# Kernel optimization log

Hardware: AMD Instinct MI355X
Metric: run time of the kernel (lower is better)

The kernel has to match this reference:

```python
import jax, jax.numpy as jnp
import numpy as np

B, L, D, H, HID = 2048, 512, 17, 8, 256  # batch, max entities, feat dim, heads, mlp hidden
SPECIAL, OUT = 9, 23  # special vector dims, policy logits (7+16)


def _lin(k, out_d, in_d, scale):
    kw, kb = jax.random.split(k)
    W = jax.random.normal(kw, (out_d, in_d), jnp.float32) * scale
    b = jax.random.normal(kb, (out_d,), jnp.float32) * 0.01
    return W, b


def setup_inputs() -> dict:
    key = jax.random.key(0)
    ks = jax.random.split(key, 16)
    # observations: row 0 holds the 9-dim special vector, rows 1..L are ragged entities
    x = jax.random.normal(ks[0], (B, L + 1, D), jnp.float32)
    lengths = jax.random.randint(ks[1], (B,), 1, L + 1)
    mask = (jnp.arange(L)[None, :] < lengths[:, None]).astype(jnp.float32)
    x = x.at[:, 1:, :].multiply(mask[:, :, None])  # zero rows mark padding
    s = 1.0 / np.sqrt(D)
    # per-head K/V projections (num_heads separate tiny Linears)
    Wk = jax.random.normal(ks[2], (H, D, D), jnp.float32) * s
    bk = jax.random.normal(ks[3], (H, D), jnp.float32) * 0.01
    Wv = jax.random.normal(ks[4], (H, D, D), jnp.float32) * s
    bv = jax.random.normal(ks[5], (H, D), jnp.float32) * 0.01
    q = jax.random.normal(ks[6], (H, D), jnp.float32)  # learned per-head queries
    Wo, bo = _lin(ks[7], D, H * D, 1.0 / np.sqrt(H * D))
    sc = 1.0 / np.sqrt(D + SPECIAL)
    pW1, pb1 = _lin(ks[8], HID, D + SPECIAL, sc)
    pW2, pb2 = _lin(ks[9], HID, HID, 1.0 / np.sqrt(HID))
    pW3, pb3 = _lin(ks[10], OUT, HID, 1.0 / np.sqrt(HID))
    vW1, vb1 = _lin(ks[11], HID, D + SPECIAL, sc)
    vW2, vb2 = _lin(ks[12], HID, HID, 1.0 / np.sqrt(HID))
    vW3, vb3 = _lin(ks[13], 1, HID, 1.0 / np.sqrt(HID))
    return dict(x=x, Wk=Wk, bk=bk, Wv=Wv, bv=bv, q=q, Wo=Wo, bo=bo,
                pW1=pW1, pb1=pb1, pW2=pW2, pb2=pb2, pW3=pW3, pb3=pb3,
                vW1=vW1, vb1=vb1, vW2=vW2, vb2=vb2, vW3=vW3, vb3=vb3)


def _mlp(h, W1, b1, W2, b2, W3, b3):
    h = jax.nn.relu(h @ W1.T + b1)
    h = jax.nn.relu(h @ W2.T + b2)
    return h @ W3.T + b3


def reference(x, Wk, bk, Wv, bv, q, Wo, bo,
              pW1, pb1, pW2, pb2, pW3, pb3,
              vW1, vb1, vW2, vb2, vW3, vb3):
    special = x[:, 0, :SPECIAL]            # [B, 9]
    seq = x[:, 1:, :]                      # [B, L, D]
    mask = jnp.sum(jnp.abs(seq), axis=-1) != 0  # [B, L] non-padded rows
    # per-head keys/values for all samples at once (batched over the head loop)
    keys = jnp.einsum('bld,hed->bhle', seq, Wk) + bk[None, :, None, :]   # [B,H,L,D]
    vals = jnp.einsum('bld,hed->bhle', seq, Wv) + bv[None, :, None, :]   # [B,H,L,D]
    scores = jnp.einsum('bhle,he->bhl', keys, q)                          # [B,H,L]
    scores = jnp.where(mask[:, None, :], scores, -1e9)
    w = jax.nn.softmax(scores, axis=-1)                                   # [B,H,L]
    agg = jnp.einsum('bhl,bhle->bhe', w, vals).reshape(x.shape[0], H * D)  # concat heads
    attn = agg @ Wo.T + bo                                                # [B, D]
    comb = jnp.concatenate([attn, special], axis=-1)                      # [B, D+9]
    logits = _mlp(comb, pW1, pb1, pW2, pb2, pW3, pb3)                     # [B, 23]
    value = _mlp(comb, vW1, vb1, vW2, vb2, vW3, vb3)                      # [B, 1]
    return logits, value
```

## Files before the change

kernel.cpp:

```cpp
#include <hip/hip_runtime.h>
#include <hip/hip_bf16.h>

#define B_ 2048
#define D_ 17
#define H_ 8
#define HID_ 256
#define OUT_ 23
#define XROW 8721
#define SEQN 8704
#define LAST4 4465151

typedef unsigned int u32;
typedef const __attribute__((address_space(1))) u32* gp1_t;
typedef __attribute__((address_space(3))) u32* lp3_t;

__device__ __forceinline__ float bclane(float v, int l) {
  return __uint_as_float(__builtin_amdgcn_readlane(__float_as_uint(v), l));
}

__device__ __forceinline__ void gload_lds16(const float4* gsrc_lane, float* lds_wave_base) {
  __builtin_amdgcn_global_load_lds((gp1_t)(const void*)gsrc_lane,
                                   (lp3_t)(void*)lds_wave_base, 16, 0, 0);
}

__global__ __launch_bounds__(256) void prep_kernel(
    const float* __restrict__ pW2, const float* __restrict__ vW2,
    const float* __restrict__ Wk, const float* __restrict__ bk,
    const float* __restrict__ q,
    float* __restrict__ pW2t, float* __restrict__ vW2t, float* __restrict__ qkc)
{
  const int bid = blockIdx.x;
  const int t = threadIdx.x;
  if (bid == 128) {
    if (t < H_ * D_) {
      const int h = t / D_, dd = t - h * D_;
      float s = 0.f;
      #pragma unroll
      for (int e = 0; e < D_; ++e) s = fmaf(Wk[h*289 + e*D_ + dd], q[h*D_ + e], s);
      qkc[h*18 + dd] = s;
    } else if (t < H_ * D_ + H_) {
      const int h = t - H_ * D_;
      float s = 0.f;
      #pragma unroll
      for (int e = 0; e < D_; ++e) s = fmaf(bk[h*D_ + e], q[h*D_ + e], s);
      qkc[h*18 + 17] = s;
    }
    return;
  }
  __shared__ float tile[32][33];
  const int m = bid >> 6, tid = bid & 63;
  const int ti = (tid >> 3) * 32, tk = (tid & 7) * 32;
  const float* src = m ? vW2 : pW2;
  float* dst = m ? vW2t : pW2t;
  const int tx = t & 31, ty = t >> 5;
  #pragma unroll
  for (int r = 0; r < 4; ++r) tile[ty + 8*r][tx] = src[(ti + ty + 8*r)*HID_ + tk + tx];
  __syncthreads();
  #pragma unroll
  for (int r = 0; r < 4; ++r) dst[(tk + ty + 8*r)*HID_ + ti + tx] = tile[tx][ty + 8*r];
}

__global__ __launch_bounds__(256, 4) void attn_comb_kernel(
    const float* __restrict__ x, const float* __restrict__ qkc,
    const float* __restrict__ Wv, const float* __restrict__ bv,
    const float* __restrict__ Wo, const float* __restrict__ bo,
    float* __restrict__ comb)
{
  __shared__ __align__(16) float s_seq[9216];
  __shared__ float s_part[4][H_][18];
  __shared__ float s_swn[136];
  __shared__ float s_agg[136];
  __shared__ float s_wp[136];

  const int t = threadIdx.x;
  const int b = blockIdx.x;
  const int w = t >> 6, lane = t & 63;
  const int hp = lane >> 4;
  const int rg = lane & 15;
  const int seq0 = b * XROW + D_;
  const int s4 = seq0 >> 2;
  const int phase = seq0 & 3;
  const float4* __restrict__ x4 = (const float4*)x;

  const float pv = x[seq0 + lane * 136];

  {
    float* dstb = s_seq + ((t & ~63) << 2);
    const int g0 = s4 + t;
    gload_lds16(x4 + g0,          dstb);
    gload_lds16(x4 + g0 + 256,    dstb + 1024);
    gload_lds16(x4 + g0 + 512,    dstb + 2048);
    gload_lds16(x4 + g0 + 768,    dstb + 3072);
    gload_lds16(x4 + g0 + 1024,   dstb + 4096);

    const unsigned long long live = __ballot(pv != 0.f) | 1ull;
    const int nr = 8 * (64 - __builtin_clzll(live));
    const int rounds = min(9, (nr * D_ + phase + 1023) >> 10);

    if (rounds > 5) gload_lds16(x4 + g0 + 1280, dstb + 5120);
    if (rounds > 6) gload_lds16(x4 + g0 + 1536, dstb + 6144);
    if (rounds > 7) gload_lds16(x4 + g0 + 1792, dstb + 7168);
    if (rounds > 8) gload_lds16(x4 + min(g0 + 2048, LAST4), dstb + 8192);
  }
  const unsigned long long live2 = __ballot(pv != 0.f) | 1ull;
  const int nrows = 8 * (64 - __builtin_clzll(live2));

  const float* q0 = qkc + (2*hp) * 18;
  float qk0[D_], qk1[D_];
  #pragma unroll
  for (int d = 0; d < D_; ++d) { qk0[d] = q0[d]; qk1[d] = q0[18 + d]; }
  const float ch0 = q0[17], ch1 = q0[35];

  __syncthreads();

  float den0 = 0.f, den1 = 0.f;
  float acc0[D_], acc1[D_];
  #pragma unroll
  for (int d = 0; d < D_; ++d) { acc0[d] = 0.f; acc1[d] = 0.f; }

  auto dorow = [&](int row) {
    const float* rp = &s_seq[phase + row * D_];
    const float f0 = rp[0],  f1 = rp[1],  f2 = rp[2],  f3 = rp[3];
    const float f4 = rp[4],  f5 = rp[5],  f6 = rp[6],  f7 = rp[7];
    const float f8 = rp[8],  f9 = rp[9],  f10 = rp[10], f11 = rp[11];
    const float f12 = rp[12], f13 = rp[13], f14 = rp[14], f15 = rp[15];
    const float f16 = rp[16];
    float sA = ch0, sB = ch1;
    sA = fmaf(qk0[0],  f0,  sA); sB = fmaf(qk1[0],  f0,  sB);
    sA = fmaf(qk0[1],  f1,  sA); sB = fmaf(qk1[1],  f1,  sB);
    sA = fmaf(qk0[2],  f2,  sA); sB = fmaf(qk1[2],  f2,  sB);
    sA = fmaf(qk0[3],  f3,  sA); sB = fmaf(qk1[3],  f3,  sB);
    sA = fmaf(qk0[4],  f4,  sA); sB = fmaf(qk1[4],  f4,  sB);
    sA = fmaf(qk0[5],  f5,  sA); sB = fmaf(qk1[5],  f5,  sB);
    sA = fmaf(qk0[6],  f6,  sA); sB = fmaf(qk1[6],  f6,  sB);
    sA = fmaf(qk0[7],  f7,  sA); sB = fmaf(qk1[7],  f7,  sB);
    sA = fmaf(qk0[8],  f8,  sA); sB = fmaf(qk1[8],  f8,  sB);
    sA = fmaf(qk0[9],  f9,  sA); sB = fmaf(qk1[9],  f9,  sB);
    sA = fmaf(qk0[10], f10, sA); sB = fmaf(qk1[10], f10, sB);
    sA = fmaf(qk0[11], f11, sA); sB = fmaf(qk1[11], f11, sB);
    sA = fmaf(qk0[12], f12, sA); sB = fmaf(qk1[12], f12, sB);
    sA = fmaf(qk0[13], f13, sA); sB = fmaf(qk1[13], f13, sB);
    sA = fmaf(qk0[14], f14, sA); sB = fmaf(qk1[14], f14, sB);
    sA = fmaf(qk0[15], f15, sA); sB = fmaf(qk1[15], f15, sB);
    sA = fmaf(qk0[16], f16, sA); sB = fmaf(qk1[16], f16, sB);
    const bool lv = (row < nrows) && (f0 != 0.f);
    const float p0 = lv ? __expf(sA) : 0.f;
    const float p1 = lv ? __expf(sB) : 0.f;
    den0 += p0; den1 += p1;
    acc0[0]  = fmaf(p0, f0,  acc0[0]);  acc1[0]  = fmaf(p1, f0,  acc1[0]);
    acc0[1]  = fmaf(p0, f1,  acc0[1]);  acc1[1]  = fmaf(p1, f1,  acc1[1]);
    acc0[2]  = fmaf(p0, f2,  acc0[2]);  acc1[2]  = fmaf(p1, f2,  acc1[2]);
    acc0[3]  = fmaf(p0, f3,  acc0[3]);  acc1[3]  = fmaf(p1, f3,  acc1[3]);
    acc0[4]  = fmaf(p0, f4,  acc0[4]);  acc1[4]  = fmaf(p1, f4,  acc1[4]);
    acc0[5]  = fmaf(p0, f5,  acc0[5]);  acc1[5]  = fmaf(p1, f5,  acc1[5]);
    acc0[6]  = fmaf(p0, f6,  acc0[6]);  acc1[6]  = fmaf(p1, f6,  acc1[6]);
    acc0[7]  = fmaf(p0, f7,  acc0[7]);  acc1[7]  = fmaf(p1, f7,  acc1[7]);
    acc0[8]  = fmaf(p0, f8,  acc0[8]);  acc1[8]  = fmaf(p1, f8,  acc1[8]);
    acc0[9]  = fmaf(p0, f9,  acc0[9]);  acc1[9]  = fmaf(p1, f9,  acc1[9]);
    acc0[10] = fmaf(p0, f10, acc0[10]); acc1[10] = fmaf(p1, f10, acc1[10]);
    acc0[11] = fmaf(p0, f11, acc0[11]); acc1[11] = fmaf(p1, f11, acc1[11]);
    acc0[12] = fmaf(p0, f12, acc0[12]); acc1[12] = fmaf(p1, f12, acc1[12]);
    acc0[13] = fmaf(p0, f13, acc0[13]); acc1[13] = fmaf(p1, f13, acc1[13]);
    acc0[14] = fmaf(p0, f14, acc0[14]); acc1[14] = fmaf(p1, f14, acc1[14]);
    acc0[15] = fmaf(p0, f15, acc0[15]); acc1[15] = fmaf(p1, f15, acc1[15]);
    acc0[16] = fmaf(p0, f16, acc0[16]); acc1[16] = fmaf(p1, f16, acc1[16]);
  };

  {
    const int s0r = w * 64;
    if (s0r < nrows) {
      dorow(s0r + rg);
      dorow(s0r + rg + 16);
      dorow(s0r + rg + 32);
      dorow(s0r + rg + 48);
    }
    const int s1r = 256 + w * 64;
    if (s1r < nrows) {
      dorow(s1r + rg);
      dorow(s1r + rg + 16);
      dorow(s1r + rg + 32);
      dorow(s1r + rg + 48);
    }
  }

  #pragma unroll
  for (int m = 1; m <= 8; m <<= 1) {
    den0 += __shfl_xor(den0, m, 64);
    den1 += __shfl_xor(den1, m, 64);
    #pragma unroll
    for (int d = 0; d < D_; ++d) {
      acc0[d] += __shfl_xor(acc0[d], m, 64);
      acc1[d] += __shfl_xor(acc1[d], m, 64);
    }
  }
  if (rg == 0) {
    float* p0p = &s_part[w][2*hp][0];
    float* p1p = &s_part[w][2*hp + 1][0];
    p0p[0] = den0; p1p[0] = den1;
    #pragma unroll
    for (int d = 0; d < D_; ++d) { p0p[1 + d] = acc0[d]; p1p[1 + d] = acc1[d]; }
  }
  __syncthreads();

  if (t < 136) {
    const int hh = t / D_, d = t - hh * D_;
    float dn = 0.f, ac = 0.f;
    #pragma unroll
    for (int ww = 0; ww < 4; ++ww) { dn += s_part[ww][hh][0]; ac += s_part[ww][hh][1 + d]; }
    s_swn[t] = ac / dn;
  }
  __syncthreads();
  if (t < 136) {
    const int hh = t / D_, e = t - hh * D_;
    float s = bv[t];
    #pragma unroll
    for (int d = 0; d < D_; ++d) s = fmaf(Wv[hh*289 + e*D_ + d], s_swn[hh*D_ + d], s);
    s_agg[t] = s;
  }
  __syncthreads();
  if (t < 136) {
    const int o = t >> 3, pt = t & 7;
    float s = 0.f;
    #pragma unroll
    for (int j = 0; j < D_; ++j) s = fmaf(Wo[o*136 + pt*D_ + j], s_agg[pt*D_ + j], s);
    s_wp[t] = s;
  }
  __syncthreads();
  if (t < D_) {
    float s = bo[t];
    #pragma unroll
    for (int pt = 0; pt < 8; ++pt) s += s_wp[t*8 + pt];
    comb[b*26 + t] = s;
  } else if (t < 26) {
    comb[b*26 + t] = x[b * XROW + (t - D_)];
  }
}

__global__ __launch_bounds__(512) void mlp_kernel(
    const float* __restrict__ comb,
    const float* __restrict__ pW1, const float* __restrict__ pb1,
    const float* __restrict__ pW2t, const float* __restrict__ pb2,
    const float* __restrict__ pW3, const float* __restrict__ pb3,
    const float* __restrict__ vW1, const float* __restrict__ vb1,
    const float* __restrict__ vW2t, const float* __restrict__ vb2,
    const float* __restrict__ vW3, const float* __restrict__ vb3,
    float* __restrict__ out)
{
  __shared__ float s_comb[4][26];
  __shared__ __align__(16) float s_red[2][3][4][HID_];
  __shared__ __align__(16) float s_h2[2][4][HID_];

  const int t = threadIdx.x;
  const int b0 = blockIdx.x * 4;
  const int p = t >> 8;
  const int kq = (t >> 6) & 3;
  const int ln = t & 63;

  if (t < 104) { const int bb = t / 26, k = t - bb*26; s_comb[bb][k] = comb[(size_t)(b0 + bb)*26 + k]; }
  __syncthreads();

  const float* W1  = p ? vW1  : pW1;   const float* B1 = p ? vb1 : pb1;
  const float* W2t = p ? vW2t : pW2t;  const float* B2 = p ? vb2 : pb2;

  float h[4];
  {
    const int i = kq * 64 + ln;
    float a[4] = {0.f, 0.f, 0.f, 0.f};
    const float* wr = W1 + i * 26;
    for (int k = 0; k < 26; ++k) {
      const float wk = wr[k];
      #pragma unroll
      for (int bb = 0; bb < 4; ++bb) a[bb] = fmaf(wk, s_comb[bb][k], a[bb]);
    }
    const float bias = B1[i];
    #pragma unroll
    for (int bb = 0; bb < 4; ++bb) h[bb] = fmaxf(a[bb] + bias, 0.f);
  }

  float4 acc[4];
  #pragma unroll
  for (int bb = 0; bb < 4; ++bb) acc[bb] = make_float4(0.f, 0.f, 0.f, 0.f);
  {
    const float* wbase = W2t + (size_t)(kq * 64) * HID_ + 4 * ln;
    #pragma unroll 8
    for (int jj = 0; jj < 64; ++jj) {
      const float4 wv = *(const float4*)(wbase + (size_t)jj * HID_);
      #pragma unroll
      for (int bb = 0; bb < 4; ++bb) {
        const float hv = bclane(h[bb], jj);
        acc[bb].x = fmaf(wv.x, hv, acc[bb].x);
        acc[bb].y = fmaf(wv.y, hv, acc[bb].y);
        acc[bb].z = fmaf(wv.z, hv, acc[bb].z);
        acc[bb].w = fmaf(wv.w, hv, acc[bb].w);
      }
    }
  }
  if (kq > 0) {
    #pragma unroll
    for (int bb = 0; bb < 4; ++bb) *(float4*)&s_red[p][kq - 1][bb][4 * ln] = acc[bb];
  }
  __syncthreads();
  if (kq == 0) {
    const float4 bias = *(const float4*)&B2[4 * ln];
    #pragma unroll
    for (int bb = 0; bb < 4; ++bb) {
      const float4 r0 = *(const float4*)&s_red[p][0][bb][4 * ln];
      const float4 r1 = *(const float4*)&s_red[p][1][bb][4 * ln];
      const float4 r2 = *(const float4*)&s_red[p][2][bb][4 * ln];
      float4 rr;
      rr.x = fmaxf(acc[bb].x + r0.x + r1.x + r2.x + bias.x, 0.f);
      rr.y = fmaxf(acc[bb].y + r0.y + r1.y + r2.y + bias.y, 0.f);
      rr.z = fmaxf(acc[bb].z + r0.z + r1.z + r2.z + bias.z, 0.f);
      rr.w = fmaxf(acc[bb].w + r0.w + r1.w + r2.w + bias.w, 0.f);
      *(float4*)&s_h2[p][bb][4 * ln] = rr;
    }
  }
  __syncthreads();

  if (t < 92) {
    const int bb = t / OUT_, o = t - bb * OUT_;
    const float4* w4 = (const float4*)(pW3 + o * HID_);
    const float4* h4 = (const float4*)&s_h2[0][bb][0];
    float s = pb3[o];
    for (int k = 0; k < 64; ++k) {
      const float4 wv = w4[k], hv = h4[k];
      s = fmaf(wv.x, hv.x, fmaf(wv.y, hv.y, fmaf(wv.z, hv.z, fmaf(wv.w, hv.w, s))));
    }
    out[(size_t)(b0 + bb) * OUT_ + o] = s;
  } else if (t >= 256 && t < 260) {
    const int bb = t - 256;
    const float4* w4 = (const float4*)vW3;
    const float4* h4 = (const float4*)&s_h2[1][bb][0];
    float s = vb3[0];
    for (int k = 0; k < 64; ++k) {
      const float4 wv = w4[k], hv = h4[k];
      s = fmaf(wv.x, hv.x, fmaf(wv.y, hv.y, fmaf(wv.z, hv.z, fmaf(wv.w, hv.w, s))));
    }
    out[(size_t)B_ * OUT_ + b0 + bb] = s;
  }
}

extern "C" void kernel_launch(void* const* d_in, const int* in_sizes, int n_in,
                              void* d_out, int out_size, void* d_ws, size_t ws_size,
                              hipStream_t stream) {
  (void)in_sizes; (void)n_in; (void)out_size; (void)ws_size;
  const float* x   = (const float*)d_in[0];
  const float* Wk  = (const float*)d_in[1];
  const float* bk  = (const float*)d_in[2];
  const float* Wv  = (const float*)d_in[3];
  const float* bv  = (const float*)d_in[4];
  const float* q   = (const float*)d_in[5];
  const float* Wo  = (const float*)d_in[6];
  const float* bo  = (const float*)d_in[7];
  const float* pW1 = (const float*)d_in[8];
  const float* pb1 = (const float*)d_in[9];
  const float* pW2 = (const float*)d_in[10];
  const float* pb2 = (const float*)d_in[11];
  const float* pW3 = (const float*)d_in[12];
  const float* pb3 = (const float*)d_in[13];
  const float* vW1 = (const float*)d_in[14];
  const float* vb1 = (const float*)d_in[15];
  const float* vW2 = (const float*)d_in[16];
  const float* vb2 = (const float*)d_in[17];
  const float* vW3 = (const float*)d_in[18];
  const float* vb3 = (const float*)d_in[19];
  float* out = (float*)d_out;

  float* pW2t = (float*)d_ws;
  float* vW2t = pW2t + (size_t)HID_ * HID_;
  float* qkc  = vW2t + (size_t)HID_ * HID_;
  float* comb = qkc + 160;

  prep_kernel<<<129, 256, 0, stream>>>(pW2, vW2, Wk, bk, q, pW2t, vW2t, qkc);
  attn_comb_kernel<<<B_, 256, 0, stream>>>(x, qkc, Wv, bv, Wo, bo, comb);
  mlp_kernel<<<B_ / 4, 512, 0, stream>>>(comb, pW1, pb1, pW2t, pb2, pW3, pb3,
                                         vW1, vb1, vW2t, vb2, vW3, vb3, out);
}
```

Before: 53.35 us.

## Fuse attention pooling and MLP heads into one kernel over 4 samples

Merges the per-sample attention kernel and the batched MLP kernel into a single kernel. Each block loops over 4 samples to compute the combined features into shared memory, then runs the policy and value MLPs serially, reusing the sequence buffer. This removes one launch and the global round trip of the combined features. In exchange, the grid shrinks fourfold, loads for successive samples are serialized without overlap, and occupancy hints change, which may reduce memory-level parallelism.

```diff
diff --git a/kernel.cpp b/kernel.cpp
--- a/kernel.cpp
+++ b/kernel.cpp
@@ -60,184 +60,10 @@
   for (int r = 0; r < 4; ++r) dst[(tk + ty + 8*r)*HID_ + ti + tx] = tile[tx][ty + 8*r];
 }
 
-__global__ __launch_bounds__(256, 4) void attn_comb_kernel(
+__global__ __launch_bounds__(256, 3) void fused_kernel(
     const float* __restrict__ x, const float* __restrict__ qkc,
     const float* __restrict__ Wv, const float* __restrict__ bv,
     const float* __restrict__ Wo, const float* __restrict__ bo,
-    float* __restrict__ comb)
-{
-  __shared__ __align__(16) float s_seq[9216];
-  __shared__ float s_part[4][H_][18];
-  __shared__ float s_swn[136];
-  __shared__ float s_agg[136];
-  __shared__ float s_wp[136];
-
-  const int t = threadIdx.x;
-  const int b = blockIdx.x;
-  const int w = t >> 6, lane = t & 63;
-  const int hp = lane >> 4;
-  const int rg = lane & 15;
-  const int seq0 = b * XROW + D_;
-  const int s4 = seq0 >> 2;
-  const int phase = seq0 & 3;
-  const float4* __restrict__ x4 = (const float4*)x;
-
-  const float pv = x[seq0 + lane * 136];
-
-  {
-    float* dstb = s_seq + ((t & ~63) << 2);
-    const int g0 = s4 + t;
-    gload_lds16(x4 + g0,          dstb);
-    gload_lds16(x4 + g0 + 256,    dstb + 1024);
-    gload_lds16(x4 + g0 + 512,    dstb + 2048);
-    gload_lds16(x4 + g0 + 768,    dstb + 3072);
-    gload_lds16(x4 + g0 + 1024,   dstb + 4096);
-
-    const unsigned long long live = __ballot(pv != 0.f) | 1ull;
-    const int nr = 8 * (64 - __builtin_clzll(live));
-    const int rounds = min(9, (nr * D_ + phase + 1023) >> 10);
-
-    if (rounds > 5) gload_lds16(x4 + g0 + 1280, dstb + 5120);
-    if (rounds > 6) gload_lds16(x4 + g0 + 1536, dstb + 6144);
-    if (rounds > 7) gload_lds16(x4 + g0 + 1792, dstb + 7168);
-    if (rounds > 8) gload_lds16(x4 + min(g0 + 2048, LAST4), dstb + 8192);
-  }
-  const unsigned long long live2 = __ballot(pv != 0.f) | 1ull;
-  const int nrows = 8 * (64 - __builtin_clzll(live2));
-
-  const float* q0 = qkc + (2*hp) * 18;
-  float qk0[D_], qk1[D_];
-  #pragma unroll
-  for (int d = 0; d < D_; ++d) { qk0[d] = q0[d]; qk1[d] = q0[18 + d]; }
-  const float ch0 = q0[17], ch1 = q0[35];
-
-  __syncthreads();
-
-  float den0 = 0.f, den1 = 0.f;
-  float acc0[D_], acc1[D_];
-  #pragma unroll
-  for (int d = 0; d < D_; ++d) { acc0[d] = 0.f; acc1[d] = 0.f; }
-
-  auto dorow = [&](int row) {
-    const float* rp = &s_seq[phase + row * D_];
-    const float f0 = rp[0],  f1 = rp[1],  f2 = rp[2],  f3 = rp[3];
-    const float f4 = rp[4],  f5 = rp[5],  f6 = rp[6],  f7 = rp[7];
-    const float f8 = rp[8],  f9 = rp[9],  f10 = rp[10], f11 = rp[11];
-    const float f12 = rp[12], f13 = rp[13], f14 = rp[14], f15 = rp[15];
-    const float f16 = rp[16];
-    float sA = ch0, sB = ch1;
-    sA = fmaf(qk0[0],  f0,  sA); sB = fmaf(qk1[0],  f0,  sB);
-    sA = fmaf(qk0[1],  f1,  sA); sB = fmaf(qk1[1],  f1,  sB);
-    sA = fmaf(qk0[2],  f2,  sA); sB = fmaf(qk1[2],  f2,  sB);
-    sA = fmaf(qk0[3],  f3,  sA); sB = fmaf(qk1[3],  f3,  sB);
-    sA = fmaf(qk0[4],  f4,  sA); sB = fmaf(qk1[4],  f4,  sB);
-    sA = fmaf(qk0[5],  f5,  sA); sB = fmaf(qk1[5],  f5,  sB);
-    sA = fmaf(qk0[6],  f6,  sA); sB = fmaf(qk1[6],  f6,  sB);
-    sA = fmaf(qk0[7],  f7,  sA); sB = fmaf(qk1[7],  f7,  sB);
-    sA = fmaf(qk0[8],  f8,  sA); sB = fmaf(qk1[8],  f8,  sB);
-    sA = fmaf(qk0[9],  f9,  sA); sB = fmaf(qk1[9],  f9,  sB);
-    sA = fmaf(qk0[10], f10, sA); sB = fmaf(qk1[10], f10, sB);
-    sA = fmaf(qk0[11], f11, sA); sB = fmaf(qk1[11], f11, sB);
-    sA = fmaf(qk0[12], f12, sA); sB = fmaf(qk1[12], f12, sB);
-    sA = fmaf(qk0[13], f13, sA); sB = fmaf(qk1[13], f13, sB);
-    sA = fmaf(qk0[14], f14, sA); sB = fmaf(qk1[14], f14, sB);
-    sA = fmaf(qk0[15], f15, sA); sB = fmaf(qk1[15], f15, sB);
-    sA = fmaf(qk0[16], f16, sA); sB = fmaf(qk1[16], f16, sB);
-    const bool lv = (row < nrows) && (f0 != 0.f);
-    const float p0 = lv ? __expf(sA) : 0.f;
-    const float p1 = lv ? __expf(sB) : 0.f;
-    den0 += p0; den1 += p1;
-    acc0[0]  = fmaf(p0, f0,  acc0[0]);  acc1[0]  = fmaf(p1, f0,  acc1[0]);
-    acc0[1]  = fmaf(p0, f1,  acc0[1]);  acc1[1]  = fmaf(p1, f1,  acc1[1]);
-    acc0[2]  = fmaf(p0, f2,  acc0[2]);  acc1[2]  = fmaf(p1, f2,  acc1[2]);
-    acc0[3]  = fmaf(p0, f3,  acc0[3]);  acc1[3]  = fmaf(p1, f3,  acc1[3]);
-    acc0[4]  = fmaf(p0, f4,  acc0[4]);  acc1[4]  = fmaf(p1, f4,  acc1[4]);
-    acc0[5]  = fmaf(p0, f5,  acc0[5]);  acc1[5]  = fmaf(p1, f5,  acc1[5]);
-    acc0[6]  = fmaf(p0, f6,  acc0[6]);  acc1[6]  = fmaf(p1, f6,  acc1[6]);
-    acc0[7]  = fmaf(p0, f7,  acc0[7]);  acc1[7]  = fmaf(p1, f7,  acc1[7]);
-    acc0[8]  = fmaf(p0, f8,  acc0[8]);  acc1[8]  = fmaf(p1, f8,  acc1[8]);
-    acc0[9]  = fmaf(p0, f9,  acc0[9]);  acc1[9]  = fmaf(p1, f9,  acc1[9]);
-    acc0[10] = fmaf(p0, f10, acc0[10]); acc1[10] = fmaf(p1, f10, acc1[10]);
-    acc0[11] = fmaf(p0, f11, acc0[11]); acc1[11] = fmaf(p1, f11, acc1[11]);
-    acc0[12] = fmaf(p0, f12, acc0[12]); acc1[12] = fmaf(p1, f12, acc1[12]);
-    acc0[13] = fmaf(p0, f13, acc0[13]); acc1[13] = fmaf(p1, f13, acc1[13]);
-    acc0[14] = fmaf(p0, f14, acc0[14]); acc1[14] = fmaf(p1, f14, acc1[14]);
-    acc0[15] = fmaf(p0, f15, acc0[15]); acc1[15] = fmaf(p1, f15, acc1[15]);
-    acc0[16] = fmaf(p0, f16, acc0[16]); acc1[16] = fmaf(p1, f16, acc1[16]);
-  };
-
-  {
-    const int s0r = w * 64;
-    if (s0r < nrows) {
-      dorow(s0r + rg);
-      dorow(s0r + rg + 16);
-      dorow(s0r + rg + 32);
-      dorow(s0r + rg + 48);
-    }
-    const int s1r = 256 + w * 64;
-    if (s1r < nrows) {
-      dorow(s1r + rg);
-      dorow(s1r + rg + 16);
-      dorow(s1r + rg + 32);
-      dorow(s1r + rg + 48);
-    }
-  }
-
-  #pragma unroll
-  for (int m = 1; m <= 8; m <<= 1) {
-    den0 += __shfl_xor(den0, m, 64);
-    den1 += __shfl_xor(den1, m, 64);
-    #pragma unroll
-    for (int d = 0; d < D_; ++d) {
-      acc0[d] += __shfl_xor(acc0[d], m, 64);
-      acc1[d] += __shfl_xor(acc1[d], m, 64);
-    }
-  }
-  if (rg == 0) {
-    float* p0p = &s_part[w][2*hp][0];
-    float* p1p = &s_part[w][2*hp + 1][0];
-    p0p[0] = den0; p1p[0] = den1;
-    #pragma unroll
-    for (int d = 0; d < D_; ++d) { p0p[1 + d] = acc0[d]; p1p[1 + d] = acc1[d]; }
-  }
-  __syncthreads();
-
-  if (t < 136) {
-    const int hh = t / D_, d = t - hh * D_;
-    float dn = 0.f, ac = 0.f;
-    #pragma unroll
-    for (int ww = 0; ww < 4; ++ww) { dn += s_part[ww][hh][0]; ac += s_part[ww][hh][1 + d]; }
-    s_swn[t] = ac / dn;
-  }
-  __syncthreads();
-  if (t < 136) {
-    const int hh = t / D_, e = t - hh * D_;
-    float s = bv[t];
-    #pragma unroll
-    for (int d = 0; d < D_; ++d) s = fmaf(Wv[hh*289 + e*D_ + d], s_swn[hh*D_ + d], s);
-    s_agg[t] = s;
-  }
-  __syncthreads();
-  if (t < 136) {
-    const int o = t >> 3, pt = t & 7;
-    float s = 0.f;
-    #pragma unroll
-    for (int j = 0; j < D_; ++j) s = fmaf(Wo[o*136 + pt*D_ + j], s_agg[pt*D_ + j], s);
-    s_wp[t] = s;
-  }
-  __syncthreads();
-  if (t < D_) {
-    float s = bo[t];
-    #pragma unroll
-    for (int pt = 0; pt < 8; ++pt) s += s_wp[t*8 + pt];
-    comb[b*26 + t] = s;
-  } else if (t < 26) {
-    comb[b*26 + t] = x[b * XROW + (t - D_)];
-  }
-}
-
-__global__ __launch_bounds__(512) void mlp_kernel(
-    const float* __restrict__ comb,
     const float* __restrict__ pW1, const float* __restrict__ pb1,
     const float* __restrict__ pW2t, const float* __restrict__ pb2,
     const float* __restrict__ pW3, const float* __restrict__ pb3,
@@ -246,97 +72,271 @@
     const float* __restrict__ vW3, const float* __restrict__ vb3,
     float* __restrict__ out)
 {
-  __shared__ float s_comb[4][26];
-  __shared__ __align__(16) float s_red[2][3][4][HID_];
-  __shared__ __align__(16) float s_h2[2][4][HID_];
+  __shared__ __align__(16) float s_seq[9216];
+  __shared__ float s_part[4][H_][18];
+  __shared__ float s_swn[136];
+  __shared__ float s_agg[136];
+  __shared__ float s_wp[136];
+  __shared__ float s_combL[4][28];
 
   const int t = threadIdx.x;
-  const int b0 = blockIdx.x * 4;
-  const int p = t >> 8;
-  const int kq = (t >> 6) & 3;
-  const int ln = t & 63;
-
-  if (t < 104) { const int bb = t / 26, k = t - bb*26; s_comb[bb][k] = comb[(size_t)(b0 + bb)*26 + k]; }
-  __syncthreads();
-
-  const float* W1  = p ? vW1  : pW1;   const float* B1 = p ? vb1 : pb1;
-  const float* W2t = p ? vW2t : pW2t;  const float* B2 = p ? vb2 : pb2;
-
-  float h[4];
-  {
-    const int i = kq * 64 + ln;
-    float a[4] = {0.f, 0.f, 0.f, 0.f};
-    const float* wr = W1 + i * 26;
-    for (int k = 0; k < 26; ++k) {
-      const float wk = wr[k];
-      #pragma unroll
-      for (int bb = 0; bb < 4; ++bb) a[bb] = fmaf(wk, s_comb[bb][k], a[bb]);
-    }
-    const float bias = B1[i];
+  const int w = t >> 6, lane = t & 63;
+  const int hp = lane >> 4;
+  const int rg = lane & 15;
+  const float4* __restrict__ x4 = (const float4*)x;
+
+  const float* q0 = qkc + (2*hp) * 18;
+  float qk0[D_], qk1[D_];
+  #pragma unroll
+  for (int d = 0; d < D_; ++d) { qk0[d] = q0[d]; qk1[d] = q0[18 + d]; }
+  const float ch0 = q0[17], ch1 = q0[35];
+
+  #pragma unroll 1
+  for (int j = 0; j < 4; ++j) {
+    const int b = blockIdx.x * 4 + j;
+    const int seq0 = b * XROW + D_;
+    const int s4 = seq0 >> 2;
+    const int phase = seq0 & 3;
+
+    const float pv = x[seq0 + lane * 136];
+
+    {
+      float* dstb = s_seq + ((t & ~63) << 2);
+      const int g0 = s4 + t;
+      gload_lds16(x4 + g0,          dstb);
+      gload_lds16(x4 + g0 + 256,    dstb + 1024);
+      gload_lds16(x4 + g0 + 512,    dstb + 2048);
+      gload_lds16(x4 + g0 + 768,    dstb + 3072);
+      gload_lds16(x4 + g0 + 1024,   dstb + 4096);
+
+      const unsigned long long live = __ballot(pv != 0.f) | 1ull;
+      const int nr = 8 * (64 - __builtin_clzll(live));
+      const int rounds = min(9, (nr * D_ + phase + 1023) >> 10);
+
+      if (rounds > 5) gload_lds16(x4 + g0 + 1280, dstb + 5120);
+      if (rounds > 6) gload_lds16(x4 + g0 + 1536, dstb + 6144);
+      if (rounds > 7) gload_lds16(x4 + g0 + 1792, dstb + 7168);
+      if (rounds > 8) gload_lds16(x4 + min(g0 + 2048, LAST4), dstb + 8192);
+    }
+    const unsigned long long live2 = __ballot(pv != 0.f) | 1ull;
+    const int nrows = 8 * (64 - __builtin_clzll(live2));
+
+    __syncthreads();
+
+    float den0 = 0.f, den1 = 0.f;
+    float acc0[D_], acc1[D_];
     #pragma unroll
-    for (int bb = 0; bb < 4; ++bb) h[bb] = fmaxf(a[bb] + bias, 0.f);
+    for (int d = 0; d < D_; ++d) { acc0[d] = 0.f; acc1[d] = 0.f; }
+
+    auto dorow = [&](int row) {
+      const float* rp = &s_seq[phase + row * D_];
+      const float f0 = rp[0],  f1 = rp[1],  f2 = rp[2],  f3 = rp[3];
+      const float f4 = rp[4],  f5 = rp[5],  f6 = rp[6],  f7 = rp[7];
+      const float f8 = rp[8],  f9 = rp[9],  f10 = rp[10], f11 = rp[11];
+      const float f12 = rp[12], f13 = rp[13], f14 = rp[14], f15 = rp[15];
+      const float f16 = rp[16];
+      float sA = ch0, sB = ch1;
+      sA = fmaf(qk0[0],  f0,  sA); sB = fmaf(qk1[0],  f0,  sB);
+      sA = fmaf(qk0[1],  f1,  sA); sB = fmaf(qk1[1],  f1,  sB);
+      sA = fmaf(qk0[2],  f2,  sA); sB = fmaf(qk1[2],  f2,  sB);
+      sA = fmaf(qk0[3],  f3,  sA); sB = fmaf(qk1[3],  f3,  sB);
+      sA = fmaf(qk0[4],  f4,  sA); sB = fmaf(qk1[4],  f4,  sB);
+      sA = fmaf(qk0[5],  f5,  sA); sB = fmaf(qk1[5],  f5,  sB);
+      sA = fmaf(qk0[6],  f6,  sA); sB = fmaf(qk1[6],  f6,  sB);
+      sA = fmaf(qk0[7],  f7,  sA); sB = fmaf(qk1[7],  f7,  sB);
+      sA = fmaf(qk0[8],  f8,  sA); sB = fmaf(qk1[8],  f8,  sB);
+      sA = fmaf(qk0[9],  f9,  sA); sB = fmaf(qk1[9],  f9,  sB);
+      sA = fmaf(qk0[10], f10, sA); sB = fmaf(qk1[10], f10, sB);
+      sA = fmaf(qk0[11], f11, sA); sB = fmaf(qk1[11], f11, sB);
+      sA = fmaf(qk0[12], f12, sA); sB = fmaf(qk1[12], f12, sB);
+      sA = fmaf(qk0[13], f13, sA); sB = fmaf(qk1[13], f13, sB);
+      sA = fmaf(qk0[14], f14, sA); sB = fmaf(qk1[14], f14, sB);
+      sA = fmaf(qk0[15], f15, sA); sB = fmaf(qk1[15], f15, sB);
+      sA = fmaf(qk0[16], f16, sA); sB = fmaf(qk1[16], f16, sB);
+      const bool lv = (row < nrows) && (f0 != 0.f);
+      const float p0 = lv ? __expf(sA) : 0.f;
+      const float p1 = lv ? __expf(sB) : 0.f;
+      den0 += p0; den1 += p1;
+      acc0[0]  = fmaf(p0, f0,  acc0[0]);  acc1[0]  = fmaf(p1, f0,  acc1[0]);
+      acc0[1]  = fmaf(p0, f1,  acc0[1]);  acc1[1]  = fmaf(p1, f1,  acc1[1]);
+      acc0[2]  = fmaf(p0, f2,  acc0[2]);  acc1[2]  = fmaf(p1, f2,  acc1[2]);
+      acc0[3]  = fmaf(p0, f3,  acc0[3]);  acc1[3]  = fmaf(p1, f3,  acc1[3]);
+      acc0[4]  = fmaf(p0, f4,  acc0[4]);  acc1[4]  = fmaf(p1, f4,  acc1[4]);
+      acc0[5]  = fmaf(p0, f5,  acc0[5]);  acc1[5]  = fmaf(p1, f5,  acc1[5]);
+      acc0[6]  = fmaf(p0, f6,  acc0[6]);  acc1[6]  = fmaf(p1, f6,  acc1[6]);
+      acc0[7]  = fmaf(p0, f7,  acc0[7]);  acc1[7]  = fmaf(p1, f7,  acc1[7]);
+      acc0[8]  = fmaf(p0, f8,  acc0[8]);  acc1[8]  = fmaf(p1, f8,  acc1[8]);
+      acc0[9]  = fmaf(p0, f9,  acc0[9]);  acc1[9]  = fmaf(p1, f9,  acc1[9]);
+      acc0[10] = fmaf(p0, f10, acc0[10]); acc1[10] = fmaf(p1, f10, acc1[10]);
+      acc0[11] = fmaf(p0, f11, acc0[11]); acc1[11] = fmaf(p1, f11, acc1[11]);
+      acc0[12] = fmaf(p0, f12, acc0[12]); acc1[12] = fmaf(p1, f12, acc1[12]);
+      acc0[13] = fmaf(p0, f13, acc0[13]); acc1[13] = fmaf(p1, f13, acc1[13]);
+      acc0[14] = fmaf(p0, f14, acc0[14]); acc1[14] = fmaf(p1, f14, acc1[14]);
+      acc0[15] = fmaf(p0, f15, acc0[15]); acc1[15] = fmaf(p1, f15, acc1[15]);
+      acc0[16] = fmaf(p0, f16, acc0[16]); acc1[16] = fmaf(p1, f16, acc1[16]);
+    };
+
+    {
+      const int s0r = w * 64;
+      if (s0r < nrows) {
+        dorow(s0r + rg);
+        dorow(s0r + rg + 16);
+        dorow(s0r + rg + 32);
+        dorow(s0r + rg + 48);
+      }
+      const int s1r = 256 + w * 64;
+      if (s1r < nrows) {
+        dorow(s1r + rg);
+        dorow(s1r + rg + 16);
+        dorow(s1r + rg + 32);
+        dorow(s1r + rg + 48);
+      }
+    }
+
+    #pragma unroll
+    for (int m = 1; m <= 8; m <<= 1) {
+      den0 += __shfl_xor(den0, m, 64);
+      den1 += __shfl_xor(den1, m, 64);
+      #pragma unroll
+      for (int d = 0; d < D_; ++d) {
+        acc0[d] += __shfl_xor(acc0[d], m, 64);
+        acc1[d] += __shfl_xor(acc1[d], m, 64);
+      }
+    }
+    if (rg == 0) {
+      float* p0p = &s_part[w][2*hp][0];
+      float* p1p = &s_part[w][2*hp + 1][0];
+      p0p[0] = den0; p1p[0] = den1;
+      #pragma unroll
+      for (int d = 0; d < D_; ++d) { p0p[1 + d] = acc0[d]; p1p[1 + d] = acc1[d]; }
+    }
+    __syncthreads();
+
+    if (t < 136) {
+      const int hh = t / D_, d = t - hh * D_;
+      float dn = 0.f, ac = 0.f;
+      #pragma unroll
+      for (int ww = 0; ww < 4; ++ww) { dn += s_part[ww][hh][0]; ac += s_part[ww][hh][1 + d]; }
+      s_swn[t] = ac / dn;
+    }
+    __syncthreads();
+    if (t < 136) {
+      const int hh = t / D_, e = t - hh * D_;
+      float s = bv[t];
+      #pragma unroll
+      for (int d = 0; d < D_; ++d) s = fmaf(Wv[hh*289 + e*D_ + d], s_swn[hh*D_ + d], s);
+      s_agg[t] = s;
+    }
+    __syncthreads();
+    if (t < 136) {
+      const int o = t >> 3, pt = t & 7;
+      float s = 0.f;
+      #pragma unroll
+      for (int jj = 0; jj < D_; ++jj) s = fmaf(Wo[o*136 + pt*D_ + jj], s_agg[pt*D_ + jj], s);
+      s_wp[t] = s;
+    }
+    __syncthreads();
+    if (t < D_) {
+      float s = bo[t];
+      #pragma unroll
+      for (int pt = 0; pt < 8; ++pt) s += s_wp[t*8 + pt];
+      s_combL[j][t] = s;
+    } else if (t < 26) {
+      s_combL[j][t] = x[b * XROW + (t - D_)];
+    }
+    __syncthreads();
   }
 
-  float4 acc[4];
+  float* s_red = s_seq;
+  float* s_h2  = s_seq + 3072;
+  const int kq = t >> 6, ln = t & 63;
+
   #pragma unroll
-  for (int bb = 0; bb < 4; ++bb) acc[bb] = make_float4(0.f, 0.f, 0.f, 0.f);
-  {
-    const float* wbase = W2t + (size_t)(kq * 64) * HID_ + 4 * ln;
-    #pragma unroll 8
-    for (int jj = 0; jj < 64; ++jj) {
-      const float4 wv = *(const float4*)(wbase + (size_t)jj * HID_);
+  for (int p = 0; p < 2; ++p) {
+    const float* W1  = p ? vW1  : pW1;   const float* B1 = p ? vb1 : pb1;
+    const float* W2t = p ? vW2t : pW2t;  const float* B2 = p ? vb2 : pb2;
+
+    float h[4];
+    {
+      float a[4] = {0.f, 0.f, 0.f, 0.f};
+      const float* wr = W1 + t * 26;
+      for (int k = 0; k < 26; ++k) {
+        const float wk = wr[k];
+        #pragma unroll
+        for (int bb = 0; bb < 4; ++bb) a[bb] = fmaf(wk, s_combL[bb][k], a[bb]);
+      }
+      const float bias = B1[t];
+      #pragma unroll
+      for (int bb = 0; bb < 4; ++bb) h[bb] = fmaxf(a[bb] + bias, 0.f);
+    }
+
+    float4 acc[4];
+    #pragma unroll
+    for (int bb = 0; bb < 4; ++bb) acc[bb] = make_float4(0.f, 0.f, 0.f, 0.f);
+    {
+      const float* wbase = W2t + (size_t)(kq * 64) * HID_ + 4 * ln;
+      #pragma unroll 8
+      for (int jj = 0; jj < 64; ++jj) {
+        const float4 wv = *(const float4*)(wbase + (size_t)jj * HID_);
+        #pragma unroll
+        for (int bb = 0; bb < 4; ++bb) {
+          const float hv = bclane(h[bb], jj);
+          acc[bb].x = fmaf(wv.x, hv, acc[bb].x);
+          acc[bb].y = fmaf(wv.y, hv, acc[bb].y);
+          acc[bb].z = fmaf(wv.z, hv, acc[bb].z);
+          acc[bb].w = fmaf(wv.w, hv, acc[bb].w);
+        }
+      }
+    }
+    if (kq > 0) {
+      #pragma unroll
+      for (int bb = 0; bb < 4; ++bb)
+        *(float4*)&s_red[((kq - 1) * 4 + bb) * HID_ + 4 * ln] = acc[bb];
+    }
+    __syncthreads();
+    if (kq == 0) {
+      const float4 bias = *(const float4*)&B2[4 * ln];
       #pragma unroll
       for (int bb = 0; bb < 4; ++bb) {
-        const float hv = bclane(h[bb], jj);
-        acc[bb].x = fmaf(wv.x, hv, acc[bb].x);
-        acc[bb].y = fmaf(wv.y, hv, acc[bb].y);
-        acc[bb].z = fmaf(wv.z, hv, acc[bb].z);
-        acc[bb].w = fmaf(wv.w, hv, acc[bb].w);
-      }
-    }
-  }
-  if (kq > 0) {
-    #pragma unroll
-    for (int bb = 0; bb < 4; ++bb) *(float4*)&s_red[p][kq - 1][bb][4 * ln] = acc[bb];
-  }
-  __syncthreads();
-  if (kq == 0) {
-    const float4 bias = *(const float4*)&B2[4 * ln];
-    #pragma unroll
-    for (int bb = 0; bb < 4; ++bb) {
-      const float4 r0 = *(const float4*)&s_red[p][0][bb][4 * ln];
-      const float4 r1 = *(const float4*)&s_red[p][1][bb][4 * ln];
-      const float4 r2 = *(const float4*)&s_red[p][2][bb][4 * ln];
-      float4 rr;
-      rr.x = fmaxf(acc[bb].x + r0.x + r1.x + r2.x + bias.x, 0.f);
-      rr.y = fmaxf(acc[bb].y + r0.y + r1.y + r2.y + bias.y, 0.f);
-      rr.z = fmaxf(acc[bb].z + r0.z + r1.z + r2.z + bias.z, 0.f);
-      rr.w = fmaxf(acc[bb].w + r0.w + r1.w + r2.w + bias.w, 0.f);
-      *(float4*)&s_h2[p][bb][4 * ln] = rr;
-    }
-  }
-  __syncthreads();
-
-  if (t < 92) {
-    const int bb = t / OUT_, o = t - bb * OUT_;
-    const float4* w4 = (const float4*)(pW3 + o * HID_);
-    const float4* h4 = (const float4*)&s_h2[0][bb][0];
-    float s = pb3[o];
-    for (int k = 0; k < 64; ++k) {
-      const float4 wv = w4[k], hv = h4[k];
-      s = fmaf(wv.x, hv.x, fmaf(wv.y, hv.y, fmaf(wv.z, hv.z, fmaf(wv.w, hv.w, s))));
-    }
-    out[(size_t)(b0 + bb) * OUT_ + o] = s;
-  } else if (t >= 256 && t < 260) {
-    const int bb = t - 256;
-    const float4* w4 = (const float4*)vW3;
-    const float4* h4 = (const float4*)&s_h2[1][bb][0];
-    float s = vb3[0];
-    for (int k = 0; k < 64; ++k) {
-      const float4 wv = w4[k], hv = h4[k];
-      s = fmaf(wv.x, hv.x, fmaf(wv.y, hv.y, fmaf(wv.z, hv.z, fmaf(wv.w, hv.w, s))));
-    }
-    out[(size_t)B_ * OUT_ + b0 + bb] = s;
+        const float4 r0 = *(const float4*)&s_red[(0 * 4 + bb) * HID_ + 4 * ln];
+        const float4 r1 = *(const float4*)&s_red[(1 * 4 + bb) * HID_ + 4 * ln];
+        const float4 r2 = *(const float4*)&s_red[(2 * 4 + bb) * HID_ + 4 * ln];
+        float4 rr;
+        rr.x = fmaxf(acc[bb].x + r0.x + r1.x + r2.x + bias.x, 0.f);
+        rr.y = fmaxf(acc[bb].y + r0.y + r1.y + r2.y + bias.y, 0.f);
+        rr.z = fmaxf(acc[bb].z + r0.z + r1.z + r2.z + bias.z, 0.f);
+        rr.w = fmaxf(acc[bb].w + r0.w + r1.w + r2.w + bias.w, 0.f);
+        *(float4*)&s_h2[bb * HID_ + 4 * ln] = rr;
+      }
+    }
+    __syncthreads();
+
+    if (p == 0) {
+      if (t < 92) {
+        const int bb = t / OUT_, o = t - bb * OUT_;
+        const float4* w4 = (const float4*)(pW3 + o * HID_);
+        const float4* h4 = (const float4*)&s_h2[bb * HID_];
+        float s = pb3[o];
+        for (int k = 0; k < 64; ++k) {
+          const float4 wv = w4[k], hv = h4[k];
+          s = fmaf(wv.x, hv.x, fmaf(wv.y, hv.y, fmaf(wv.z, hv.z, fmaf(wv.w, hv.w, s))));
+        }
+        out[(size_t)(blockIdx.x * 4 + bb) * OUT_ + o] = s;
+      }
+    } else {
+      if (t < 4) {
+        const int bb = t;
+        const float4* w4 = (const float4*)vW3;
+        const float4* h4 = (const float4*)&s_h2[bb * HID_];
+        float s = vb3[0];
+        for (int k = 0; k < 64; ++k) {
+          const float4 wv = w4[k], hv = h4[k];
+          s = fmaf(wv.x, hv.x, fmaf(wv.y, hv.y, fmaf(wv.z, hv.z, fmaf(wv.w, hv.w, s))));
+        }
+        out[(size_t)B_ * OUT_ + blockIdx.x * 4 + bb] = s;
+      }
+    }
+    __syncthreads();
   }
 }
 
@@ -369,10 +369,9 @@
   float* pW2t = (float*)d_ws;
   float* vW2t = pW2t + (size_t)HID_ * HID_;
   float* qkc  = vW2t + (size_t)HID_ * HID_;
-  float* comb = qkc + 160;
 
   prep_kernel<<<129, 256, 0, stream>>>(pW2, vW2, Wk, bk, q, pW2t, vW2t, qkc);
-  attn_comb_kernel<<<B_, 256, 0, stream>>>(x, qkc, Wv, bv, Wo, bo, comb);
-  mlp_kernel<<<B_ / 4, 512, 0, stream>>>(comb, pW1, pb1, pW2t, pb2, pW3, pb3,
-                                         vW1, vb1, vW2t, vb2, vW3, vb3, out);
-}
+  fused_kernel<<<B_ / 4, 256, 0, stream>>>(x, qkc, Wv, bv, Wo, bo,
+                                           pW1, pb1, pW2t, pb2, pW3, pb3,
+                                           vW1, vb1, vW2t, vb2, vW3, vb3, out);
+}
```

Result: slower. 61.70 us (+15.7%).
